# Kernel optimization log

Hardware: AMD Instinct MI355X
Metric: run time of the kernel (lower is better)

Reference implementation:

```python
import jax, jax.numpy as jnp
import numpy as np

B, S, HID = 2, 2048, 2048
HQ, HKV, D = 32, 4, 128
EPS = 1e-6
SCALE = D ** -0.5


def _rms_norm(x, w):
    # per-head RMSNorm over last dim, computed in fp32 like the torch module
    xf = x.astype(jnp.float32)
    var = jnp.mean(xf * xf, axis=-1, keepdims=True)
    return (w * (xf * jax.lax.rsqrt(var + EPS))).astype(x.dtype)


def _rotate_half(x):
    x1, x2 = jnp.split(x, 2, axis=-1)
    return jnp.concatenate([-x2, x1], axis=-1)


def setup_inputs() -> dict:
    key = jax.random.key(0)
    ks = jax.random.split(key, 8)
    hidden_states = jax.random.normal(ks[0], (B, S, HID), dtype=jnp.float32)
    # RoPE tables (HF Qwen style, theta=1e6)
    inv_freq = 1.0 / (1e6 ** (np.arange(0, D, 2, dtype=np.float32) / D))
    t = np.arange(S, dtype=np.float32)
    freqs = np.outer(t, inv_freq)                      # [S, D/2]
    emb = np.concatenate([freqs, freqs], axis=-1)      # [S, D]
    cos = jnp.asarray(np.cos(emb))
    sin = jnp.asarray(np.sin(emb))
    sd = HID ** -0.5
    wq = jax.random.normal(ks[1], (HID, HQ * D), dtype=jnp.float32) * sd
    wk = jax.random.normal(ks[2], (HID, HKV * D), dtype=jnp.float32) * sd
    wv = jax.random.normal(ks[3], (HID, HKV * D), dtype=jnp.float32) * sd
    wo = jax.random.normal(ks[4], (HQ * D, HID), dtype=jnp.float32) * ((HQ * D) ** -0.5)
    q_norm_w = jnp.ones((D,), dtype=jnp.float32)
    k_norm_w = jnp.ones((D,), dtype=jnp.float32)
    return {"hidden_states": hidden_states, "cos": cos, "sin": sin,
            "wq": wq, "wk": wk, "wv": wv, "wo": wo,
            "q_norm_w": q_norm_w, "k_norm_w": k_norm_w}


def reference(hidden_states, cos, sin, wq, wk, wv, wo, q_norm_w, k_norm_w):
    b, s, _ = hidden_states.shape
    # QKV projection (no bias)
    q = (hidden_states @ wq).reshape(b, s, HQ, D)
    k = (hidden_states @ wk).reshape(b, s, HKV, D)
    v = (hidden_states @ wv).reshape(b, s, HKV, D)
    # per-head RMSNorm on q, k
    q = _rms_norm(q, q_norm_w)
    k = _rms_norm(k, k_norm_w)
    # RoPE: cos/sin [s, D] -> broadcast over batch and heads
    c = cos[None, :, None, :]
    sn = sin[None, :, None, :]
    q = q * c + _rotate_half(q) * sn
    k = k * c + _rotate_half(k) * sn
    # [b, h, s, d]
    q = q.transpose(0, 2, 1, 3)
    k = k.transpose(0, 2, 1, 3)
    v = v.transpose(0, 2, 1, 3)
    # GQA: repeat kv heads to match query heads
    groups = HQ // HKV
    k = jnp.repeat(k, groups, axis=1)
    v = jnp.repeat(v, groups, axis=1)
    # causal SDPA (prefill)
    scores = jnp.einsum('bhqd,bhkd->bhqk', q, k) * SCALE
    causal = jnp.tril(jnp.ones((s, s), dtype=bool))
    scores = jnp.where(causal[None, None], scores, jnp.finfo(scores.dtype).min)
    attn = jax.nn.softmax(scores, axis=-1)
    out = jnp.einsum('bhqk,bhkd->bhqd', attn, v)
    out = out.transpose(0, 2, 1, 3).reshape(b, s, HQ * D)
    return out @ wo
```

## Files before the change

### kernel.cpp

```cpp
#include <hip/hip_runtime.h>
#include <hip/hip_bf16.h>
#include <stdint.h>

typedef __bf16 bf16;
typedef __bf16 bf16x4 __attribute__((ext_vector_type(4)));
typedef __bf16 bf16x8 __attribute__((ext_vector_type(8)));
typedef float floatx4 __attribute__((ext_vector_type(4)));

#define MFMA16(a, b, c) __builtin_amdgcn_mfma_f32_16x16x32_bf16((a), (b), (c), 0, 0, 0)

static __device__ __forceinline__ void async_load16(const bf16* g, bf16* l) {
    __builtin_amdgcn_global_load_lds(
        (const __attribute__((address_space(1))) uint32_t*)(const void*)g,
        (__attribute__((address_space(3))) uint32_t*)(void*)l,
        16, 0, 0);
}

static __device__ __forceinline__ bf16x8 load8(const bf16* p) {
    return *(const bf16x8*)p;
}
static __device__ __forceinline__ bf16x8 load8(const float* p) {
    const float4 a = *(const float4*)p;
    const float4 b = *(const float4*)(p + 4);
    bf16x8 r;
    r[0] = (bf16)a.x; r[1] = (bf16)a.y; r[2] = (bf16)a.z; r[3] = (bf16)a.w;
    r[4] = (bf16)b.x; r[5] = (bf16)b.y; r[6] = (bf16)b.z; r[7] = (bf16)b.w;
    return r;
}

__global__ __launch_bounds__(256) void f2b(const float* __restrict__ in,
                                           bf16* __restrict__ out) {
    const size_t i = ((size_t)blockIdx.x * 256 + threadIdx.x) * 8;
    *(bf16x8*)&out[i] = load8(in + i);
}

__global__ __launch_bounds__(256) void transposeF2B(const float* __restrict__ in,
                                                    bf16* __restrict__ out,
                                                    int R, int C) {
    __shared__ float t[32][33];
    const int c0 = blockIdx.x * 32, r0 = blockIdx.y * 32;
    const int tx = threadIdx.x & 31, ty = threadIdx.x >> 5;
#pragma unroll
    for (int i = 0; i < 4; i++)
        t[ty + i * 8][tx] = in[(size_t)(r0 + ty + i * 8) * C + c0 + tx];
    __syncthreads();
#pragma unroll
    for (int i = 0; i < 4; i++)
        out[(size_t)(c0 + ty + i * 8) * R + r0 + tx] = (bf16)t[tx][ty + i * 8];
}

__global__ __launch_bounds__(256) void gemm_qkv(const bf16* __restrict__ A,
                                                const bf16* __restrict__ BT,
                                                bf16* __restrict__ Q,
                                                bf16* __restrict__ K2,
                                                bf16* __restrict__ Vt) {
    constexpr int K = 2048;
    __shared__ __attribute__((aligned(16))) bf16 As[128 * 32];
    __shared__ __attribute__((aligned(16))) bf16 Bs[128 * 32];
    const int tid = threadIdx.x;
    const int wave = tid >> 6, lane = tid & 63;
    const int quad = lane >> 4, l16 = lane & 15;
    const int m0 = blockIdx.y * 128, n0 = blockIdx.x * 128;
    const int wr = (wave >> 1) * 64, wc = (wave & 1) * 64;

    floatx4 acc[4][4] = {};

    const bf16* gA = A + (size_t)(m0 + wave * 32 + (lane >> 2)) * K + (lane & 3) * 8;
    const bf16* gB = BT + (size_t)(n0 + wave * 32 + (lane >> 2)) * K + (lane & 3) * 8;

    for (int k0 = 0; k0 < K; k0 += 32) {
        async_load16(gA + k0, &As[(wave * 32) * 32]);
        async_load16(gA + k0 + 16 * (size_t)K, &As[(wave * 32 + 16) * 32]);
        async_load16(gB + k0, &Bs[(wave * 32) * 32]);
        async_load16(gB + k0 + 16 * (size_t)K, &Bs[(wave * 32 + 16) * 32]);
        __syncthreads();

        bf16x8 af[4], bfr[4];
#pragma unroll
        for (int i = 0; i < 4; i++)
            af[i] = *(const bf16x8*)&As[(wr + i * 16 + l16) * 32 + quad * 8];
#pragma unroll
        for (int j = 0; j < 4; j++)
            bfr[j] = *(const bf16x8*)&Bs[(wc + j * 16 + l16) * 32 + quad * 8];
#pragma unroll
        for (int i = 0; i < 4; i++)
#pragma unroll
            for (int j = 0; j < 4; j++)
                acc[i][j] = MFMA16(af[i], bfr[j], acc[i][j]);
        __syncthreads();
    }

    const int region = (n0 >= 4608) ? 2 : (n0 >= 4096 ? 1 : 0);
#pragma unroll
    for (int i = 0; i < 4; i++) {
#pragma unroll
        for (int j = 0; j < 4; j++) {
            const int row = m0 + wr + i * 16 + quad * 4;
            const int col = n0 + wc + j * 16 + l16;
            if (region == 0) {
#pragma unroll
                for (int r = 0; r < 4; r++)
                    Q[(size_t)(row + r) * 4096 + col] = (bf16)acc[i][j][r];
            } else if (region == 1) {
#pragma unroll
                for (int r = 0; r < 4; r++)
                    K2[(size_t)(row + r) * 512 + (col - 4096)] = (bf16)acc[i][j][r];
            } else {
                bf16x4 t;
#pragma unroll
                for (int r = 0; r < 4; r++) t[r] = (bf16)acc[i][j][r];
                *(bf16x4*)&Vt[(size_t)(col - 4608) * 4096 + row] = t;
            }
        }
    }
}

__global__ __launch_bounds__(256) void gemm_o(const bf16* __restrict__ A,
                                              const bf16* __restrict__ BT,
                                              float* __restrict__ C) {
    constexpr int K = 4096, N = 2048;
    __shared__ __attribute__((aligned(16))) bf16 As[128 * 32];
    __shared__ __attribute__((aligned(16))) bf16 Bs[128 * 32];
    const int tid = threadIdx.x;
    const int wave = tid >> 6, lane = tid & 63;
    const int quad = lane >> 4, l16 = lane & 15;
    const int m0 = blockIdx.y * 128, n0 = blockIdx.x * 128;
    const int wr = (wave >> 1) * 64, wc = (wave & 1) * 64;

    floatx4 acc[4][4] = {};

    const bf16* gA = A + (size_t)(m0 + wave * 32 + (lane >> 2)) * K + (lane & 3) * 8;
    const bf16* gB = BT + (size_t)(n0 + wave * 32 + (lane >> 2)) * K + (lane & 3) * 8;

    for (int k0 = 0; k0 < K; k0 += 32) {
        async_load16(gA + k0, &As[(wave * 32) * 32]);
        async_load16(gA + k0 + 16 * (size_t)K, &As[(wave * 32 + 16) * 32]);
        async_load16(gB + k0, &Bs[(wave * 32) * 32]);
        async_load16(gB + k0 + 16 * (size_t)K, &Bs[(wave * 32 + 16) * 32]);
        __syncthreads();

        bf16x8 af[4], bfr[4];
#pragma unroll
        for (int i = 0; i < 4; i++)
            af[i] = *(const bf16x8*)&As[(wr + i * 16 + l16) * 32 + quad * 8];
#pragma unroll
        for (int j = 0; j < 4; j++)
            bfr[j] = *(const bf16x8*)&Bs[(wc + j * 16 + l16) * 32 + quad * 8];
#pragma unroll
        for (int i = 0; i < 4; i++)
#pragma unroll
            for (int j = 0; j < 4; j++)
                acc[i][j] = MFMA16(af[i], bfr[j], acc[i][j]);
        __syncthreads();
    }

#pragma unroll
    for (int i = 0; i < 4; i++) {
#pragma unroll
        for (int j = 0; j < 4; j++) {
            const int row = m0 + wr + i * 16 + quad * 4;
            const int col = n0 + wc + j * 16 + l16;
#pragma unroll
            for (int r = 0; r < 4; r++)
                C[(size_t)(row + r) * N + col] = acc[i][j][r];
        }
    }
}

__global__ __launch_bounds__(256) void rmsrope(bf16* __restrict__ x,
                                               const float* __restrict__ w,
                                               const float* __restrict__ cosb,
                                               const float* __restrict__ sinb,
                                               int nh, int S) {
    const int lane = threadIdx.x & 63;
    const int row = blockIdx.x * 4 + (threadIdx.x >> 6);
    const int s = (row / nh) % S;
    bf16* p = x + (size_t)row * 128;
    float x1 = (float)p[lane];
    float x2 = (float)p[lane + 64];
    float ssq = x1 * x1 + x2 * x2;
#pragma unroll
    for (int m = 1; m < 64; m <<= 1) ssq += __shfl_xor(ssq, m);
    const float r = rsqrtf(ssq * (1.0f / 128.0f) + 1e-6f);
    const float y1 = w[lane] * x1 * r;
    const float y2 = w[lane + 64] * x2 * r;
    const float c1 = cosb[s * 128 + lane];
    const float s1 = sinb[s * 128 + lane];
    const float c2 = cosb[s * 128 + lane + 64];
    const float s2 = sinb[s * 128 + lane + 64];
    p[lane] = (bf16)(y1 * c1 - y2 * s1);
    p[lane + 64] = (bf16)(y2 * c2 + y1 * s2);
}

__global__ __launch_bounds__(512, 4) void attn(bf16* QO,
                                               const bf16* __restrict__ Km,
                                               const bf16* __restrict__ Vt,
                                               int S) {
    __shared__ __attribute__((aligned(16))) bf16 Kl[2][64 * 128];
    __shared__ __attribute__((aligned(16))) bf16 Vl[2][128 * 64];
    __shared__ __attribute__((aligned(16))) bf16 Pl[8][16 * 40];

    const int tid = threadIdx.x, wave = tid >> 6, lane = tid & 63;
    const int quad = lane >> 4, l16 = lane & 15;
    const int h = blockIdx.y, b = blockIdx.z;
    const int kvh = h >> 3;
    const float scale = 0.08838834764831845f;

    const bf16* Kg = Km + (size_t)b * S * 512 + kvh * 128;
    const bf16* Vg = Vt + (size_t)kvh * 128 * 4096 + (size_t)b * S;

    const int krow0 = wave * 8 + (lane >> 4);
    const int krow1 = wave * 8 + 4 + (lane >> 4);
    const bf16* kSrc0 = Kg + (size_t)krow0 * 512 + (((lane & 15) ^ (krow0 & 7)) << 3);
    const bf16* kSrc1 = Kg + (size_t)krow1 * 512 + (((lane & 15) ^ (krow1 & 7)) << 3);
    const int vrow0 = wave * 16 + (lane >> 3);
    const int vrow1 = wave * 16 + 8 + (lane >> 3);
    const bf16* vSrc0 = Vg + (size_t)vrow0 * 4096 + (((lane & 7) ^ (vrow0 & 7)) << 3);
    const bf16* vSrc1 = Vg + (size_t)vrow1 * 4096 + (((lane & 7) ^ (vrow1 & 7)) << 3);

#define STAGE(buf, kk)                                                  \
    do {                                                                \
        bf16* kb_ = &Kl[buf][(wave * 8) * 128];                         \
        bf16* vb_ = &Vl[buf][(wave * 16) * 64];                         \
        async_load16(kSrc0 + (size_t)(kk) * 512, kb_);                  \
        async_load16(kSrc1 + (size_t)(kk) * 512, kb_ + 4 * 128);        \
        async_load16(vSrc0 + (kk), vb_);                                \
        async_load16(vSrc1 + (kk), vb_ + 8 * 64);                       \
    } while (0)

    bf16* pw = &Pl[wave][0];

#pragma unroll
    for (int half = 0; half < 2; half++) {
        const int qt = half ? (15 - blockIdx.x) : blockIdx.x;
        const int qb = qt * 128 + wave * 16;

        bf16x8 qf[4];
        {
            const bf16* qrow = QO + (size_t)(b * S + qb + l16) * 4096 + h * 128 + quad * 8;
#pragma unroll
            for (int c = 0; c < 4; c++) qf[c] = *(const bf16x8*)(qrow + c * 32);
        }

        floatx4 o_acc[8] = {};
        float l_i[4] = {0.f, 0.f, 0.f, 0.f};

        const int nt = 2 * (qt + 1);
        STAGE(0, 0);

        for (int kt = 0; kt < nt; ++kt) {
            const int k0 = kt * 64;
            const int cur = kt & 1;
            if (kt + 1 < nt) {
                STAGE(cur ^ 1, (kt + 1) * 64);
                asm volatile("s_waitcnt vmcnt(4)" ::: "memory");
            } else {
                asm volatile("s_waitcnt vmcnt(0)" ::: "memory");
            }
            __builtin_amdgcn_s_barrier();
            __builtin_amdgcn_sched_barrier(0);

            if (k0 <= qb + 15) {
                const bf16* kl = &Kl[cur][0];
                const bf16* vl = &Vl[cur][0];

                floatx4 sc[4] = {};
#pragma unroll
                for (int c = 0; c < 4; c++) {
                    const int slot = ((c * 4 + quad) ^ (l16 & 7)) << 3;
#pragma unroll
                    for (int m = 0; m < 4; m++) {
                        const bf16x8 kf = *(const bf16x8*)&kl[(l16 + 16 * m) * 128 + slot];
                        sc[m] = MFMA16(qf[c], kf, sc[m]);
                    }
                }

#pragma unroll
                for (int ks = 0; ks < 2; ks++) {
                    const int kb = k0 + ks * 32;
                    if (kb > qb + 15) continue;
                    const floatx4 s0 = sc[2 * ks], s1 = sc[2 * ks + 1];
                    if (kb + 31 > qb) {
#pragma unroll
                        for (int r = 0; r < 4; r++) {
                            const int qi = qb + quad * 4 + r;
                            const float p0 = (kb + l16 > qi) ? 0.f : __expf(s0[r] * scale);
                            const float p1 = (kb + 16 + l16 > qi) ? 0.f : __expf(s1[r] * scale);
                            l_i[r] += p0 + p1;
                            pw[(quad * 4 + r) * 40 + l16] = (bf16)p0;
                            pw[(quad * 4 + r) * 40 + l16 + 16] = (bf16)p1;
                        }
                    } else {
#pragma unroll
                        for (int r = 0; r < 4; r++) {
                            const float p0 = __expf(s0[r] * scale);
                            const float p1 = __expf(s1[r] * scale);
                            l_i[r] += p0 + p1;
                            pw[(quad * 4 + r) * 40 + l16] = (bf16)p0;
                            pw[(quad * 4 + r) * 40 + l16 + 16] = (bf16)p1;
                        }
                    }
                    const bf16x8 pa = *(const bf16x8*)&pw[l16 * 40 + quad * 8];
#pragma unroll
                    for (int c = 0; c < 8; c++) {
                        const int vps = ((ks * 4 + quad) ^ (l16 & 7)) << 3;
                        const bf16x8 vf = *(const bf16x8*)&vl[(c * 16 + l16) * 64 + vps];
                        o_acc[c] = MFMA16(pa, vf, o_acc[c]);
                    }
                }
            }
            __builtin_amdgcn_s_barrier();
        }

#pragma unroll
        for (int r = 0; r < 4; r++) {
            float l = l_i[r];
            l += __shfl_xor(l, 1);
            l += __shfl_xor(l, 2);
            l += __shfl_xor(l, 4);
            l += __shfl_xor(l, 8);
            const float inv = (l > 0.f) ? 1.0f / l : 0.f;
            const size_t orow = (size_t)(b * S + qb + quad * 4 + r) * 4096 + h * 128;
#pragma unroll
            for (int c = 0; c < 8; c++)
                QO[orow + c * 16 + l16] = (bf16)(o_acc[c][r] * inv);
        }
    }
#undef STAGE
}

template <typename TA, typename TB, typename TC>
__global__ __launch_bounds__(256) void gemm_bn(const TA* __restrict__ A,
                                               const TB* __restrict__ B,
                                               TC* __restrict__ C,
                                               int M, int N, int K) {
    __shared__ __attribute__((aligned(16))) bf16 As[128 * 32];
    __shared__ __attribute__((aligned(16))) bf16 Bs[128 * 32];
    const int tid = threadIdx.x;
    const int wave = tid >> 6, lane = tid & 63;
    const int quad = lane >> 4, l16 = lane & 15;
    const int m0 = blockIdx.y * 128, n0 = blockIdx.x * 128;
    const int wr = (wave >> 1) * 64, wc = (wave & 1) * 64;
    floatx4 acc[4][4] = {};
    const int r0 = tid >> 2;
    const int kc = (tid & 3) * 8;
    const TA* gA0 = A + (size_t)(m0 + r0) * K + kc;
    const TA* gA1 = A + (size_t)(m0 + 64 + r0) * K + kc;
    const int kr = tid & 31;
    const int nc8 = (tid >> 5) * 8;
    const TB* gB = B + (size_t)kr * N + n0 + nc8;
    for (int k0 = 0; k0 < K; k0 += 32) {
        const bf16x8 a0 = load8(gA0 + k0);
        const bf16x8 a1 = load8(gA1 + k0);
        const TB* gBk = gB + (size_t)k0 * N;
        const bf16x8 b0 = load8(gBk);
        const bf16x8 b1 = load8(gBk + 64);
        __syncthreads();
        *(bf16x8*)&As[r0 * 32 + kc] = a0;
        *(bf16x8*)&As[(64 + r0) * 32 + kc] = a1;
#pragma unroll
        for (int j = 0; j < 8; j++) {
            Bs[(nc8 + j) * 32 + kr] = b0[j];
            Bs[(nc8 + 64 + j) * 32 + kr] = b1[j];
        }
        __syncthreads();
        bf16x8 af[4], bfr[4];
#pragma unroll
        for (int i = 0; i < 4; i++)
            af[i] = *(const bf16x8*)&As[(wr + i * 16 + l16) * 32 + quad * 8];
#pragma unroll
        for (int j = 0; j < 4; j++)
            bfr[j] = *(const bf16x8*)&Bs[(wc + j * 16 + l16) * 32 + quad * 8];
#pragma unroll
        for (int i = 0; i < 4; i++)
#pragma unroll
            for (int j = 0; j < 4; j++)
                acc[i][j] = MFMA16(af[i], bfr[j], acc[i][j]);
    }
#pragma unroll
    for (int i = 0; i < 4; i++) {
#pragma unroll
        for (int j = 0; j < 4; j++) {
            const int row = m0 + wr + i * 16 + quad * 4;
            const int col = n0 + wc + j * 16 + l16;
#pragma unroll
            for (int r = 0; r < 4; r++)
                C[(size_t)(row + r) * N + col] = (TC)acc[i][j][r];
        }
    }
}

__global__ __launch_bounds__(256) void attn_fb(bf16* QO,
                                               const bf16* __restrict__ Km,
                                               const bf16* __restrict__ Vm,
                                               int S) {
    __shared__ __attribute__((aligned(16))) bf16 Kl[32 * 136];
    __shared__ __attribute__((aligned(16))) bf16 Vl[128 * 40];
    __shared__ __attribute__((aligned(16))) bf16 Pl[4][16 * 40];
    const int tid = threadIdx.x, wave = tid >> 6, lane = tid & 63;
    const int quad = lane >> 4, l16 = lane & 15;
    const int q0 = blockIdx.x * 64;
    const int h = blockIdx.y, b = blockIdx.z;
    const int kvh = h >> 3;
    const int q_base = q0 + wave * 16;
    const float scale = 0.08838834764831845f;
    bf16x8 qf[4];
    {
        const bf16* qrow = QO + (size_t)(b * S + q_base + l16) * 4096 + h * 128 + quad * 8;
#pragma unroll
        for (int c = 0; c < 4; c++) qf[c] = *(const bf16x8*)(qrow + c * 32);
    }
    floatx4 o_acc[8] = {};
    float l_i[4] = {0.f, 0.f, 0.f, 0.f};
    const int kend = q0 + 64;
    for (int k0 = 0; k0 < kend; k0 += 32) {
#pragma unroll
        for (int it = 0; it < 2; ++it) {
            const int cc = tid + it * 256;
            const int row = cc >> 4;
            const int off = (cc & 15) * 8;
            const size_t gidx = (size_t)(b * S + k0 + row) * 512 + kvh * 128 + off;
            const bf16x8 kv = *(const bf16x8*)&Km[gidx];
            const bf16x8 vv = *(const bf16x8*)&Vm[gidx];
            *(bf16x8*)&Kl[row * 136 + off] = kv;
#pragma unroll
            for (int j = 0; j < 8; j++) Vl[(off + j) * 40 + row] = vv[j];
        }
        __syncthreads();
        if (k0 <= q_base + 15) {
            floatx4 sc0 = {}, sc1 = {};
#pragma unroll
            for (int c = 0; c < 4; c++) {
                bf16x8 b0 = *(const bf16x8*)&Kl[l16 * 136 + c * 32 + quad * 8];
                bf16x8 b1 = *(const bf16x8*)&Kl[(l16 + 16) * 136 + c * 32 + quad * 8];
                sc0 = MFMA16(qf[c], b0, sc0);
                sc1 = MFMA16(qf[c], b1, sc1);
            }
            const bool edge = (k0 + 31 > q_base);
            bf16* pw = &Pl[wave][0];
#pragma unroll
            for (int r = 0; r < 4; r++) {
                const int qi = q_base + quad * 4 + r;
                const bool mk0 = edge && (k0 + l16 > qi);
                const bool mk1 = edge && (k0 + 16 + l16 > qi);
                const float p0 = mk0 ? 0.f : __expf(sc0[r] * scale);
                const float p1 = mk1 ? 0.f : __expf(sc1[r] * scale);
                l_i[r] += p0 + p1;
                pw[(quad * 4 + r) * 40 + l16] = (bf16)p0;
                pw[(quad * 4 + r) * 40 + l16 + 16] = (bf16)p1;
            }
            const bf16x8 pa = *(const bf16x8*)&pw[l16 * 40 + quad * 8];
#pragma unroll
            for (int c = 0; c < 8; c++) {
                const bf16x8 vf = *(const bf16x8*)&Vl[(c * 16 + l16) * 40 + quad * 8];
                o_acc[c] = MFMA16(pa, vf, o_acc[c]);
            }
        }
        __syncthreads();
    }
#pragma unroll
    for (int r = 0; r < 4; r++) {
        float l = l_i[r];
        l += __shfl_xor(l, 1);
        l += __shfl_xor(l, 2);
        l += __shfl_xor(l, 4);
        l += __shfl_xor(l, 8);
        const float inv = (l > 0.f) ? 1.0f / l : 0.f;
        const size_t orow = (size_t)(b * S + q_base + quad * 4 + r) * 4096 + h * 128;
#pragma unroll
        for (int c = 0; c < 8; c++)
            QO[orow + c * 16 + l16] = (bf16)(o_acc[c][r] * inv);
    }
}

extern "C" void kernel_launch(void* const* d_in, const int* in_sizes, int n_in,
                              void* d_out, int out_size, void* d_ws, size_t ws_size,
                              hipStream_t stream) {
    const float* hidden = (const float*)d_in[0];
    const float* cosb = (const float*)d_in[1];
    const float* sinb = (const float*)d_in[2];
    const float* wq = (const float*)d_in[3];
    const float* wk = (const float*)d_in[4];
    const float* wv = (const float*)d_in[5];
    const float* wo = (const float*)d_in[6];
    const float* qnw = (const float*)d_in[7];
    const float* knw = (const float*)d_in[8];
    float* out = (float*)d_out;

    constexpr int B = 2, S = 2048, HID = 2048, HQ = 32, HKV = 4, D = 128;
    constexpr int M = B * S;
    constexpr int NQ = HQ * D;
    constexpr int NKV = HKV * D;
    constexpr int NQKV = NQ + 2 * NKV;

    const size_t need = ((size_t)NQKV * HID + (size_t)HID * NQ +
                         (size_t)M * NQ + 2 * (size_t)M * NKV) * sizeof(bf16);

    if (ws_size >= need) {
        bf16* p = (bf16*)d_ws;
        bf16* wqkvT = p; p += (size_t)NQKV * HID;
        bf16* X = p;     p += (size_t)HID * NQ;
        bf16* Qb = p;    p += (size_t)M * NQ;
        bf16* Kb = p;    p += (size_t)M * NKV;
        bf16* Vt = p;    p += (size_t)NKV * M;

        transposeF2B<<<dim3(NQ / 32, HID / 32), 256, 0, stream>>>(wq, wqkvT, HID, NQ);
        transposeF2B<<<dim3(NKV / 32, HID / 32), 256, 0, stream>>>(wk, wqkvT + (size_t)NQ * HID, HID, NKV);
        transposeF2B<<<dim3(NKV / 32, HID / 32), 256, 0, stream>>>(wv, wqkvT + (size_t)(NQ + NKV) * HID, HID, NKV);

        f2b<<<dim3((M * HID) / (256 * 8)), 256, 0, stream>>>(hidden, X);

        gemm_qkv<<<dim3(NQKV / 128, M / 128), 256, 0, stream>>>(X, wqkvT, Qb, Kb, Vt);

        rmsrope<<<dim3(M * HQ / 4), 256, 0, stream>>>(Qb, qnw, cosb, sinb, HQ, S);
        rmsrope<<<dim3(M * HKV / 4), 256, 0, stream>>>(Kb, knw, cosb, sinb, HKV, S);

        attn<<<dim3(S / 256, HQ, B), 512, 0, stream>>>(Qb, Kb, Vt, S);

        transposeF2B<<<dim3(HID / 32, NQ / 32), 256, 0, stream>>>(wo, X, NQ, HID);
        gemm_o<<<dim3(HID / 128, M / 128), 256, 0, stream>>>(Qb, X, out);
    } else {
        bf16* p = (bf16*)d_ws;
        bf16* Qb = p;  p += (size_t)M * NQ;
        bf16* Kb = p;  p += (size_t)M * NKV;
        bf16* Vb = p;  p += (size_t)M * NKV;

        gemm_bn<float, float, bf16><<<dim3(NQ / 128, M / 128), 256, 0, stream>>>(hidden, wq, Qb, M, NQ, HID);
        gemm_bn<float, float, bf16><<<dim3(NKV / 128, M / 128), 256, 0, stream>>>(hidden, wk, Kb, M, NKV, HID);
        gemm_bn<float, float, bf16><<<dim3(NKV / 128, M / 128), 256, 0, stream>>>(hidden, wv, Vb, M, NKV, HID);
        rmsrope<<<dim3(M * HQ / 4), 256, 0, stream>>>(Qb, qnw, cosb, sinb, HQ, S);
        rmsrope<<<dim3(M * HKV / 4), 256, 0, stream>>>(Kb, knw, cosb, sinb, HKV, S);
        attn_fb<<<dim3(S / 64, HQ, B), 256, 0, stream>>>(Qb, Kb, Vb, S);
        gemm_bn<bf16, float, float><<<dim3(HID / 128, M / 128), 256, 0, stream>>>(Qb, wo, out, M, HID, NQ);
    }
}
```

Baseline: 500.1 us.

## Double GEMM K-tile to 64 with XOR-swizzled LDS layout

Both the QKV and output-projection GEMMs now stage 64-wide K slices instead of 32, which halves the number of barrier pairs per tile. The async global-to-LDS loads permute 16-byte chunks by XOR with the row index, and the fragment reads apply the matching swizzle to avoid LDS bank conflicts. The cost is double the shared memory per block, which may reduce occupancy.

```diff
diff --git a/kernel.cpp b/kernel.cpp
--- a/kernel.cpp
+++ b/kernel.cpp
@@ -55,8 +55,8 @@
                                                 bf16* __restrict__ K2,
                                                 bf16* __restrict__ Vt) {
     constexpr int K = 2048;
-    __shared__ __attribute__((aligned(16))) bf16 As[128 * 32];
-    __shared__ __attribute__((aligned(16))) bf16 Bs[128 * 32];
+    __shared__ __attribute__((aligned(16))) bf16 As[128 * 64];
+    __shared__ __attribute__((aligned(16))) bf16 Bs[128 * 64];
     const int tid = threadIdx.x;
     const int wave = tid >> 6, lane = tid & 63;
     const int quad = lane >> 4, l16 = lane & 15;
@@ -65,28 +65,41 @@
 
     floatx4 acc[4][4] = {};
 
-    const bf16* gA = A + (size_t)(m0 + wave * 32 + (lane >> 2)) * K + (lane & 3) * 8;
-    const bf16* gB = BT + (size_t)(n0 + wave * 32 + (lane >> 2)) * K + (lane & 3) * 8;
-
-    for (int k0 = 0; k0 < K; k0 += 32) {
-        async_load16(gA + k0, &As[(wave * 32) * 32]);
-        async_load16(gA + k0 + 16 * (size_t)K, &As[(wave * 32 + 16) * 32]);
-        async_load16(gB + k0, &Bs[(wave * 32) * 32]);
-        async_load16(gB + k0 + 16 * (size_t)K, &Bs[(wave * 32 + 16) * 32]);
-        __syncthreads();
-
-        bf16x8 af[4], bfr[4];
-#pragma unroll
-        for (int i = 0; i < 4; i++)
-            af[i] = *(const bf16x8*)&As[(wr + i * 16 + l16) * 32 + quad * 8];
-#pragma unroll
-        for (int j = 0; j < 4; j++)
-            bfr[j] = *(const bf16x8*)&Bs[(wc + j * 16 + l16) * 32 + quad * 8];
-#pragma unroll
-        for (int i = 0; i < 4; i++)
+    const int wbase = wave * 32;
+    const bf16* aSrc[4]; const bf16* bSrc[4];
+#pragma unroll
+    for (int j = 0; j < 4; j++) {
+        const int r = wbase + 8 * j + (lane >> 3);
+        aSrc[j] = A + (size_t)(m0 + r) * K + (((lane & 7) ^ (r & 7)) << 3);
+        bSrc[j] = BT + (size_t)(n0 + r) * K + (((lane & 7) ^ (r & 7)) << 3);
+    }
+    bf16* aDst = &As[wbase * 64];
+    bf16* bDst = &Bs[wbase * 64];
+
+    for (int k0 = 0; k0 < K; k0 += 64) {
+#pragma unroll
+        for (int j = 0; j < 4; j++) {
+            async_load16(aSrc[j] + k0, aDst + j * 8 * 64);
+            async_load16(bSrc[j] + k0, bDst + j * 8 * 64);
+        }
+        __syncthreads();
+
+#pragma unroll
+        for (int ks = 0; ks < 2; ks++) {
+            const int slot = ((ks * 4 + quad) ^ (l16 & 7)) << 3;
+            bf16x8 af[4], bfr[4];
+#pragma unroll
+            for (int i = 0; i < 4; i++)
+                af[i] = *(const bf16x8*)&As[(wr + i * 16 + l16) * 64 + slot];
 #pragma unroll
             for (int j = 0; j < 4; j++)
-                acc[i][j] = MFMA16(af[i], bfr[j], acc[i][j]);
+                bfr[j] = *(const bf16x8*)&Bs[(wc + j * 16 + l16) * 64 + slot];
+#pragma unroll
+            for (int i = 0; i < 4; i++)
+#pragma unroll
+                for (int j = 0; j < 4; j++)
+                    acc[i][j] = MFMA16(af[i], bfr[j], acc[i][j]);
+        }
         __syncthreads();
     }
 
@@ -119,8 +132,8 @@
                                               const bf16* __restrict__ BT,
                                               float* __restrict__ C) {
     constexpr int K = 4096, N = 2048;
-    __shared__ __attribute__((aligned(16))) bf16 As[128 * 32];
-    __shared__ __attribute__((aligned(16))) bf16 Bs[128 * 32];
+    __shared__ __attribute__((aligned(16))) bf16 As[128 * 64];
+    __shared__ __attribute__((aligned(16))) bf16 Bs[128 * 64];
     const int tid = threadIdx.x;
     const int wave = tid >> 6, lane = tid & 63;
     const int quad = lane >> 4, l16 = lane & 15;
@@ -129,28 +142,41 @@
 
     floatx4 acc[4][4] = {};
 
-    const bf16* gA = A + (size_t)(m0 + wave * 32 + (lane >> 2)) * K + (lane & 3) * 8;
-    const bf16* gB = BT + (size_t)(n0 + wave * 32 + (lane >> 2)) * K + (lane & 3) * 8;
-
-    for (int k0 = 0; k0 < K; k0 += 32) {
-        async_load16(gA + k0, &As[(wave * 32) * 32]);
-        async_load16(gA + k0 + 16 * (size_t)K, &As[(wave * 32 + 16) * 32]);
-        async_load16(gB + k0, &Bs[(wave * 32) * 32]);
-        async_load16(gB + k0 + 16 * (size_t)K, &Bs[(wave * 32 + 16) * 32]);
-        __syncthreads();
-
-        bf16x8 af[4], bfr[4];
-#pragma unroll
-        for (int i = 0; i < 4; i++)
-            af[i] = *(const bf16x8*)&As[(wr + i * 16 + l16) * 32 + quad * 8];
-#pragma unroll
-        for (int j = 0; j < 4; j++)
-            bfr[j] = *(const bf16x8*)&Bs[(wc + j * 16 + l16) * 32 + quad * 8];
-#pragma unroll
-        for (int i = 0; i < 4; i++)
+    const int wbase = wave * 32;
+    const bf16* aSrc[4]; const bf16* bSrc[4];
+#pragma unroll
+    for (int j = 0; j < 4; j++) {
+        const int r = wbase + 8 * j + (lane >> 3);
+        aSrc[j] = A + (size_t)(m0 + r) * K + (((lane & 7) ^ (r & 7)) << 3);
+        bSrc[j] = BT + (size_t)(n0 + r) * K + (((lane & 7) ^ (r & 7)) << 3);
+    }
+    bf16* aDst = &As[wbase * 64];
+    bf16* bDst = &Bs[wbase * 64];
+
+    for (int k0 = 0; k0 < K; k0 += 64) {
+#pragma unroll
+        for (int j = 0; j < 4; j++) {
+            async_load16(aSrc[j] + k0, aDst + j * 8 * 64);
+            async_load16(bSrc[j] + k0, bDst + j * 8 * 64);
+        }
+        __syncthreads();
+
+#pragma unroll
+        for (int ks = 0; ks < 2; ks++) {
+            const int slot = ((ks * 4 + quad) ^ (l16 & 7)) << 3;
+            bf16x8 af[4], bfr[4];
+#pragma unroll
+            for (int i = 0; i < 4; i++)
+                af[i] = *(const bf16x8*)&As[(wr + i * 16 + l16) * 64 + slot];
 #pragma unroll
             for (int j = 0; j < 4; j++)
-                acc[i][j] = MFMA16(af[i], bfr[j], acc[i][j]);
+                bfr[j] = *(const bf16x8*)&Bs[(wc + j * 16 + l16) * 64 + slot];
+#pragma unroll
+            for (int i = 0; i < 4; i++)
+#pragma unroll
+                for (int j = 0; j < 4; j++)
+                    acc[i][j] = MFMA16(af[i], bfr[j], acc[i][j]);
+        }
         __syncthreads();
     }
 
```

New measurement: 465.0 us. 7.0% less time.
